# Kernel tuning notes

Measured on AMD Instinct MI355X. Metric: run time of the kernel, lower is better.

Reference implementation:

```python
import jax, jax.numpy as jnp
import numpy as np

B, S, D, H = 2, 2048, 1024, 16
HD = D // H  # head_dim = 64


def _rope(t, cos, sin):
    # t: (B, H, S, HD); cos/sin: (S, HD//2) -> rotate interleaved pairs
    t2 = t.reshape(*t.shape[:-1], HD // 2, 2)
    t1, t2_ = t2[..., 0], t2[..., 1]
    c = cos[None, None, :, :]
    s = sin[None, None, :, :]
    out = jnp.stack([t1 * c - t2_ * s, t1 * s + t2_ * c], axis=-1)
    return out.reshape(t.shape)


def setup_inputs() -> dict:
    key = jax.random.key(0)
    ks = jax.random.split(key, 5)
    x = jax.random.normal(ks[0], (B, S, D), dtype=jnp.float32)
    attn_mask = jnp.tril(jnp.ones((S, S), dtype=bool))  # causal
    # standard RoPE angles: pos * inv_freq
    inv_freq = 1.0 / (10000.0 ** (jnp.arange(0, HD, 2, dtype=jnp.float32) / HD))
    freqs = jnp.arange(S, dtype=jnp.float32)[:, None] * inv_freq[None, :]  # (S, HD//2)
    std = 1.0 / np.sqrt(D)
    w_qkv = jax.random.normal(ks[1], (3 * D, D), dtype=jnp.float32) * std
    b_qkv = jnp.zeros((3 * D,), dtype=jnp.float32)
    w_proj = jax.random.normal(ks[2], (D, D), dtype=jnp.float32) * std
    b_proj = jnp.zeros((D,), dtype=jnp.float32)
    return {"x": x, "attn_mask": attn_mask, "freqs": freqs,
            "w_qkv": w_qkv, "b_qkv": b_qkv, "w_proj": w_proj, "b_proj": b_proj}


def reference(x, attn_mask, freqs, w_qkv, b_qkv, w_proj, b_proj):
    # QKV projection: (B,S,D) -> (B,S,3D), split per einops pattern (three, H, HD)
    qkv = x @ w_qkv.T + b_qkv
    qkv = qkv.reshape(B, S, 3, H, HD)
    q = jnp.transpose(qkv[:, :, 0], (0, 2, 1, 3))  # (B,H,S,HD)
    k = jnp.transpose(qkv[:, :, 1], (0, 2, 1, 3))
    v = jnp.transpose(qkv[:, :, 2], (0, 2, 1, 3))
    cos, sin = jnp.cos(freqs), jnp.sin(freqs)
    q = _rope(q, cos, sin)
    k = _rope(k, cos, sin)
    scale = 1.0 / np.sqrt(HD)
    scores = jnp.einsum("bhqd,bhkd->bhqk", q, k) * scale  # (B,H,S,S)
    scores = jnp.where(attn_mask[None, None, :, :], scores, jnp.finfo(scores.dtype).min)
    attn = jax.nn.softmax(scores, axis=-1)
    out = jnp.einsum("bhqk,bhkd->bhqd", attn, v)  # (B,H,S,HD)
    out = jnp.transpose(out, (0, 2, 1, 3)).reshape(B, S, D)
    return out @ w_proj.T + b_proj
```

## Files before the change

### kernel.cpp

```cpp
#include <hip/hip_runtime.h>

#define S_LEN 2048
#define NH 16
#define HD 64
#define DMODEL 1024

typedef __bf16 bf16x8 __attribute__((ext_vector_type(8)));
typedef float floatx4 __attribute__((ext_vector_type(4)));
typedef short short8 __attribute__((ext_vector_type(8)));

__device__ inline unsigned short f2bf(float f) {
    union { float f; unsigned u; } v; v.f = f;
    unsigned u = v.u;
    unsigned r = (u + 0x7FFFu + ((u >> 16) & 1u)) >> 16;
    return (unsigned short)r;
}

__device__ __forceinline__ void gload_lds16(const void* g, void* l) {
    __builtin_amdgcn_global_load_lds(
        (const __attribute__((address_space(1))) unsigned int*)g,
        (__attribute__((address_space(3))) unsigned int*)l, 16, 0, 0);
}

#define WAITV_BAR(N) do { \
    asm volatile("s_waitcnt vmcnt(" #N ")\n\ts_barrier" ::: "memory"); \
    __builtin_amdgcn_sched_barrier(0); \
} while (0)

__device__ __forceinline__ void cvt4(const float4* __restrict__ src,
                                     uint2* __restrict__ dst, int i) {
    float4 v = src[i];
    union { unsigned short u[4]; uint2 d; } o;
    o.u[0] = f2bf(v.x); o.u[1] = f2bf(v.y); o.u[2] = f2bf(v.z); o.u[3] = f2bf(v.w);
    dst[i] = o.d;
}

__global__ __launch_bounds__(256) void prep_kernel(
    const float* __restrict__ x, const float* __restrict__ wq,
    const float* __restrict__ wp, const float* __restrict__ freqs,
    unsigned short* __restrict__ xb, unsigned short* __restrict__ wqb,
    unsigned short* __restrict__ wpb, float2* __restrict__ cs)
{
    const int tid = blockIdx.x * 256 + threadIdx.x;
    const int nth = gridDim.x * 256;
    for (int i = tid; i < (4096 * 1024) / 4; i += nth) cvt4((const float4*)x, (uint2*)xb, i);
    for (int i = tid; i < (3072 * 1024) / 4; i += nth) cvt4((const float4*)wq, (uint2*)wqb, i);
    for (int i = tid; i < (1024 * 1024) / 4; i += nth) cvt4((const float4*)wp, (uint2*)wpb, i);
    for (int i = tid; i < S_LEN * 32; i += nth) {
        const float f = freqs[i];
        float2 c; c.x = cosf(f); c.y = sinf(f);
        cs[i] = c;
    }
}

#define SROW(r) (((r) & 3) ^ (((r) >> 2) & 3))

#define QKV_STAGE(bi, kk) do { \
    unsigned short* dA_ = smem + (bi) * 8192; \
    unsigned short* dB_ = dA_ + 4096; \
    gload_lds16(ag + (kk),               dA_ + wv * 512); \
    gload_lds16(ag + 64 * DMODEL + (kk), dA_ + 2048 + wv * 512); \
    gload_lds16(bg + (kk),               dB_ + wv * 512); \
    gload_lds16(bg + 64 * DMODEL + (kk), dB_ + 2048 + wv * 512); \
} while (0)

#define QKV_COMPUTE(bi) do { \
    const unsigned short* sA_ = smem + (bi) * 8192; \
    const unsigned short* sB_ = sA_ + 4096; \
    bf16x8 af[4]; \
    _Pragma("unroll") for (int m_ = 0; m_ < 4; m_++) af[m_] = *(const bf16x8*)&sA_[aoff[m_]]; \
    _Pragma("unroll") for (int n_ = 0; n_ < 4; n_++) { \
        bf16x8 bf = *(const bf16x8*)&sB_[boff[n_]]; \
        _Pragma("unroll") for (int m_ = 0; m_ < 4; m_++) \
            acc[m_][n_] = __builtin_amdgcn_mfma_f32_16x16x32_bf16(af[m_], bf, acc[m_][n_], 0, 0, 0); \
    } \
} while (0)

__global__ __launch_bounds__(256, 3) void qkv_gemm_kernel(
    const unsigned short* __restrict__ xb, const unsigned short* __restrict__ wqb,
    const float* __restrict__ bias, const float2* __restrict__ cs,
    unsigned short* __restrict__ qb, unsigned short* __restrict__ kb,
    unsigned short* __restrict__ vb)
{
    __shared__ __align__(16) unsigned short smem[24576];

    const int t = threadIdx.x;
    const int v = (blockIdx.x & 7) * 96 + (blockIdx.x >> 3);
    const int mbase = (v / 24) * 128;
    const int nbase = (v % 24) * 128;
    const int wv = t >> 6, lane = t & 63;
    const int quad = lane >> 4, l16 = lane & 15;
    const int wr = wv >> 1, wc = wv & 1;

    floatx4 acc[4][4];
    #pragma unroll
    for (int m = 0; m < 4; m++)
        #pragma unroll
        for (int n = 0; n < 4; n++)
            #pragma unroll
            for (int r = 0; r < 4; r++) acc[m][n][r] = 0.f;

    const int srow = t >> 2;
    const int schunk = (t & 3) ^ SROW(srow);
    const unsigned short* ag = xb + (size_t)(mbase + srow) * DMODEL + schunk * 8;
    const unsigned short* bg = wqb + (size_t)(nbase + srow) * DMODEL + schunk * 8;

    const int Sl = SROW(l16);
    int aoff[4], boff[4];
    #pragma unroll
    for (int m = 0; m < 4; m++) aoff[m] = (wr * 64 + m * 16 + l16) * 32 + (quad ^ Sl) * 8;
    #pragma unroll
    for (int n = 0; n < 4; n++) boff[n] = (wc * 64 + n * 16 + l16) * 32 + (quad ^ Sl) * 8;

    QKV_STAGE(0, 0);
    QKV_STAGE(1, 32);
    for (int tb = 0; tb < 30; tb += 3) {
        WAITV_BAR(4); QKV_STAGE(2, (tb + 2) * 32); QKV_COMPUTE(0);
        WAITV_BAR(4); QKV_STAGE(0, (tb + 3) * 32); QKV_COMPUTE(1);
        WAITV_BAR(4); QKV_STAGE(1, (tb + 4) * 32); QKV_COMPUTE(2);
    }
    WAITV_BAR(4); QKV_COMPUTE(0);
    WAITV_BAR(0); QKV_COMPUTE(1);

    const int part = nbase >> 10;
    const int bidx = mbase >> 11;
    const int s0   = mbase & 2047;

    if (part == 2) {
        unsigned short* Vt = smem;
        const int hb = (nbase & 1023) >> 6;
        float bvv[4];
        #pragma unroll
        for (int nt = 0; nt < 4; nt++) bvv[nt] = bias[nbase + wc * 64 + nt * 16 + l16];
        #pragma unroll
        for (int shalf = 0; shalf < 2; shalf++) {
            __syncthreads();
            if (wr == shalf) {
                #pragma unroll
                for (int nt = 0; nt < 4; nt++) {
                    const int hdl = wc * 64 + nt * 16 + l16;
                    #pragma unroll
                    for (int m = 0; m < 4; m++)
                        #pragma unroll
                        for (int r = 0; r < 4; r++)
                            Vt[hdl * 72 + m * 16 + quad * 4 + r] = f2bf(acc[m][nt][r] + bvv[nt]);
                }
            }
            __syncthreads();
            const int hdl = t & 127, sp = t >> 7;
            const size_t bh2 = (size_t)bidx * NH + hb + (hdl >> 6);
            #pragma unroll
            for (int c = 0; c < 4; c++) {
                const int sl0 = (sp * 4 + c) * 8;
                const int sg = s0 + shalf * 64 + sl0;
                short8 vv = *(const short8*)&Vt[hdl * 72 + sl0];
                *(short8*)&vb[((bh2 * 256 + (sg >> 3)) * 64 + (hdl & 63)) * 8] = vv;
            }
        }
    } else {
        const size_t bhb = (size_t)bidx * NH;
        const int odd = l16 & 1;
        #pragma unroll
        for (int nt = 0; nt < 4; nt++) {
            const int n_ = nbase + wc * 64 + nt * 16 + l16;
            const int hd = n_ & 63;
            const size_t bh = bhb + ((n_ & 1023) >> 6);
            const float bvv = bias[n_];
            const int ci = (nt * 16 + l16) >> 1;
            #pragma unroll
            for (int m = 0; m < 4; m++) {
                #pragma unroll
                for (int r = 0; r < 4; r++) {
                    const int s = s0 + wr * 64 + m * 16 + quad * 4 + r;
                    float val = acc[m][nt][r] + bvv;
                    float other = __shfl_xor(val, 1, 64);
                    const float2 csv = cs[(size_t)s * 32 + ci];
                    float outv = odd ? fmaf(other, csv.y, val * csv.x)
                                     : fmaf(-other, csv.y, val * csv.x);
                    if (part == 0) {
                        qb[(bh * S_LEN + s) * HD + hd] = f2bf(outv * 0.125f);
                    } else {
                        kb[((bh * 8 + (hd >> 3)) * (size_t)S_LEN + s) * 8 + (hd & 7)] = f2bf(outv);
                    }
                }
            }
        }
    }
}

__global__ __launch_bounds__(512, 4) void attn_kernel(
    const unsigned short* __restrict__ qb, const unsigned short* __restrict__ kb,
    const unsigned short* __restrict__ vbk, unsigned short* __restrict__ ao)
{
    __shared__ __align__(16) unsigned short Ks[2][8 * 512];
    __shared__ __align__(16) unsigned short Vt[2][8 * 512];
    __shared__ __align__(16) unsigned short Pw[8][16 * 72];

    const int t = threadIdx.x;
    const int wv = t >> 6, lane = t & 63, quad = lane >> 4, l16 = lane & 15;
    const int qp = 15 - (blockIdx.x >> 5);
    const int qbase = qp * 128;
    const int bhid = blockIdx.x & 31;
    const int h = bhid & 15, b = bhid >> 4;
    const size_t bh = (size_t)b * NH + h;
    const unsigned short* qg  = qb + bh * S_LEN * HD;
    const unsigned short* kgB = kb + bh * 8 * S_LEN * 8;
    const unsigned short* vgB = vbk + bh * 256 * 64 * 8;

    bf16x8 qf[2];
    {
        const unsigned short* q0 = qg + (size_t)(qbase + wv * 16 + l16) * HD;
        qf[0] = *(const bf16x8*)&q0[quad * 8];
        qf[1] = *(const bf16x8*)&q0[32 + quad * 8];
    }

    bf16x8 ones;
    {
        union { short8 s; bf16x8 v; } o;
        for (int j = 0; j < 8; j++) o.s[j] = 0x3F80;
        ones = o.v;
    }

    floatx4 lfr = {0.f, 0.f, 0.f, 0.f};
    floatx4 Ofr[4];
    for (int nt = 0; nt < 4; nt++)
        for (int r = 0; r < 4; r++) Ofr[nt][r] = 0.f;

    const int ntiles = (qbase >> 6) + 2;

#define ATTN_STAGE(bufi, kt_) do { \
    const int kb_ = (kt_) * 64; \
    const unsigned short* g0 = kgB + ((size_t)wv * S_LEN + kb_ + lane) * 8; \
    gload_lds16(g0, &Ks[bufi][wv * 512]); \
    const unsigned short* g1 = vgB + ((size_t)((kb_ >> 3) + wv) * 64 + lane) * 8; \
    gload_lds16(g1, &Vt[bufi][wv * 512]); \
} while (0)

#define ATTN_COMPUTE(bufi, kt_) do { \
    const int kbase = (kt_) * 64; \
    float pex[4][4]; \
    __builtin_amdgcn_s_setprio(1); \
    _Pragma("unroll") for (int sub = 0; sub < 4; sub++) { \
        bf16x8 kf0 = *(const bf16x8*)&Ks[bufi][(0 * 4 + quad) * 512 + (sub * 16 + l16) * 8]; \
        bf16x8 kf1 = *(const bf16x8*)&Ks[bufi][(1 * 4 + quad) * 512 + (sub * 16 + l16) * 8]; \
        floatx4 sacc = {0.f, 0.f, 0.f, 0.f}; \
        sacc = __builtin_amdgcn_mfma_f32_16x16x32_bf16(kf0, qf[0], sacc, 0, 0, 0); \
        sacc = __builtin_amdgcn_mfma_f32_16x16x32_bf16(kf1, qf[1], sacc, 0, 0, 0); \
        _Pragma("unroll") for (int r = 0; r < 4; r++) pex[sub][r] = sacc[r]; \
    } \
    __builtin_amdgcn_s_setprio(0); \
    if (kbase + 63 > qbase + wv * 16) {            \
        const int q = qbase + wv * 16 + l16; \
        _Pragma("unroll") for (int sub = 0; sub < 4; sub++) \
            _Pragma("unroll") for (int r = 0; r < 4; r++) { \
                const int key = kbase + sub * 16 + quad * 4 + r; \
                if (key > q) pex[sub][r] = -1e30f; \
            } \
    } \
    _Pragma("unroll") for (int sub = 0; sub < 4; sub++) { \
        union { unsigned short s[4]; uint2 u; } pk; \
        _Pragma("unroll") for (int r = 0; r < 4; r++) pk.s[r] = f2bf(__expf(pex[sub][r])); \
        *(uint2*)&Pw[wv][l16 * 72 + sub * 16 + quad * 4] = pk.u; \
    } \
    { \
        bf16x8 pf0 = *(const bf16x8*)&Pw[wv][l16 * 72 + quad * 8]; \
        bf16x8 pf1 = *(const bf16x8*)&Pw[wv][l16 * 72 + 32 + quad * 8]; \
        __builtin_amdgcn_s_setprio(1); \
        lfr = __builtin_amdgcn_mfma_f32_16x16x32_bf16(ones, pf0, lfr, 0, 0, 0); \
        lfr = __builtin_amdgcn_mfma_f32_16x16x32_bf16(ones, pf1, lfr, 0, 0, 0); \
        _Pragma("unroll") for (int nt = 0; nt < 4; nt++) { \
            bf16x8 v0 = *(const bf16x8*)&Vt[bufi][(0 * 4 + quad) * 512 + (nt * 16 + l16) * 8]; \
            bf16x8 v1 = *(const bf16x8*)&Vt[bufi][(1 * 4 + quad) * 512 + (nt * 16 + l16) * 8]; \
            Ofr[nt] = __builtin_amdgcn_mfma_f32_16x16x32_bf16(pf0, v0, Ofr[nt], 0, 0, 0); \
            Ofr[nt] = __builtin_amdgcn_mfma_f32_16x16x32_bf16(pf1, v1, Ofr[nt], 0, 0, 0); \
        } \
        __builtin_amdgcn_s_setprio(0); \
    } \
} while (0)

    ATTN_STAGE(0, 0);
    __syncthreads();
    for (int kt = 0; kt < ntiles; ) {
        if (kt + 1 < ntiles) ATTN_STAGE(1, kt + 1);
        ATTN_COMPUTE(0, kt);
        kt++;
        if (kt >= ntiles) break;
        __syncthreads();
        if (kt + 1 < ntiles) ATTN_STAGE(0, kt + 1);
        ATTN_COMPUTE(1, kt);
        kt++;
        if (kt >= ntiles) break;
        __syncthreads();
    }

    float linv[4];
    #pragma unroll
    for (int r = 0; r < 4; r++) {
        float lq = __shfl(lfr[0], (lane & 48) | (quad * 4 + r), 64);
        linv[r] = 1.f / lq;
    }
    #pragma unroll
    for (int nt = 0; nt < 4; nt++)
        #pragma unroll
        for (int r = 0; r < 4; r++) {
            const int s = qbase + wv * 16 + quad * 4 + r;
            ao[((size_t)b * S_LEN + s) * DMODEL + h * HD + nt * 16 + l16] =
                f2bf(Ofr[nt][r] * linv[r]);
        }
#undef ATTN_STAGE
#undef ATTN_COMPUTE
}

#define PROJ_STAGE(bi, kk) do { \
    unsigned short* dA_ = smem + (bi) * 6144; \
    unsigned short* dB_ = dA_ + 4096; \
    gload_lds16(ag + (kk),               dA_ + wv * 512); \
    gload_lds16(ag + 64 * DMODEL + (kk), dA_ + 2048 + wv * 512); \
    gload_lds16(bg + (kk),               dB_ + wv * 512); \
} while (0)

#define PROJ_COMPUTE(bi) do { \
    const unsigned short* sA_ = smem + (bi) * 6144; \
    const unsigned short* sB_ = sA_ + 4096; \
    bf16x8 af[4]; \
    _Pragma("unroll") for (int m_ = 0; m_ < 4; m_++) af[m_] = *(const bf16x8*)&sA_[aoff[m_]]; \
    _Pragma("unroll") for (int n_ = 0; n_ < 2; n_++) { \
        bf16x8 bf = *(const bf16x8*)&sB_[boff[n_]]; \
        _Pragma("unroll") for (int m_ = 0; m_ < 4; m_++) \
            acc[m_][n_] = __builtin_amdgcn_mfma_f32_16x16x32_bf16(af[m_], bf, acc[m_][n_], 0, 0, 0); \
    } \
} while (0)

__global__ __launch_bounds__(256, 3) void proj_kernel(
    const unsigned short* __restrict__ a, const unsigned short* __restrict__ wpb,
    const float* __restrict__ bias, float* __restrict__ out)
{
    __shared__ __align__(16) unsigned short smem[18432];

    const int t = threadIdx.x;
    const int v = (blockIdx.x & 7) * 64 + (blockIdx.x >> 3);
    const int mbase = (v >> 4) * 128;
    const int nbase = (v & 15) * 64;
    const int wv = t >> 6, lane = t & 63, quad = lane >> 4, l16 = lane & 15;
    const int wr = wv >> 1, wc = wv & 1;

    floatx4 acc[4][2];
    #pragma unroll
    for (int m = 0; m < 4; m++)
        #pragma unroll
        for (int n = 0; n < 2; n++)
            #pragma unroll
            for (int r = 0; r < 4; r++) acc[m][n][r] = 0.f;

    const int srow = t >> 2;
    const int schunk = (t & 3) ^ SROW(srow);
    const unsigned short* ag = a + (size_t)(mbase + srow) * DMODEL + schunk * 8;
    const unsigned short* bg = wpb + (size_t)(nbase + srow) * DMODEL + schunk * 8;

    const int Sl = SROW(l16);
    int aoff[4], boff[2];
    #pragma unroll
    for (int m = 0; m < 4; m++) aoff[m] = (wr * 64 + m * 16 + l16) * 32 + (quad ^ Sl) * 8;
    #pragma unroll
    for (int n = 0; n < 2; n++) boff[n] = (wc * 32 + n * 16 + l16) * 32 + (quad ^ Sl) * 8;

    PROJ_STAGE(0, 0);
    PROJ_STAGE(1, 32);
    for (int tb = 0; tb < 30; tb += 3) {
        WAITV_BAR(3); PROJ_STAGE(2, (tb + 2) * 32); PROJ_COMPUTE(0);
        WAITV_BAR(3); PROJ_STAGE(0, (tb + 3) * 32); PROJ_COMPUTE(1);
        WAITV_BAR(3); PROJ_STAGE(1, (tb + 4) * 32); PROJ_COMPUTE(2);
    }
    WAITV_BAR(3); PROJ_COMPUTE(0);
    WAITV_BAR(0); PROJ_COMPUTE(1);

    #pragma unroll
    for (int n = 0; n < 2; n++) {
        const int nn = nbase + wc * 32 + n * 16 + l16;
        const float bvv = bias[nn];
        #pragma unroll
        for (int m = 0; m < 4; m++)
            #pragma unroll
            for (int r = 0; r < 4; r++)
                out[(size_t)(mbase + wr * 64 + m * 16 + quad * 4 + r) * DMODEL + nn] =
                    acc[m][n][r] + bvv;
    }
}

extern "C" void kernel_launch(void* const* d_in, const int* in_sizes, int n_in,
                              void* d_out, int out_size, void* d_ws, size_t ws_size,
                              hipStream_t stream) {
    const float* x      = (const float*)d_in[0];
    const float* freqs  = (const float*)d_in[2];
    const float* w_qkv  = (const float*)d_in[3];
    const float* b_qkv  = (const float*)d_in[4];
    const float* w_proj = (const float*)d_in[5];
    const float* b_proj = (const float*)d_in[6];
    float* out = (float*)d_out;

    unsigned short* ws = (unsigned short*)d_ws;
    const size_t HSZ = (size_t)2 * NH * S_LEN * HD;
    unsigned short* qb  = ws;
    unsigned short* kb  = ws + HSZ;
    unsigned short* vb  = ws + 2 * HSZ;
    unsigned short* ao  = ws + 3 * HSZ;
    unsigned short* xb  = ws + 4 * HSZ;
    unsigned short* wqb = xb + (size_t)4096 * 1024;
    unsigned short* wpb = wqb + (size_t)3072 * 1024;
    float2* cs = (float2*)(wpb + (size_t)1024 * 1024);

    prep_kernel<<<2048, 256, 0, stream>>>(x, w_qkv, w_proj, freqs, xb, wqb, wpb, cs);
    qkv_gemm_kernel<<<768, 256, 0, stream>>>(xb, wqb, b_qkv, cs, qb, kb, vb);
    attn_kernel<<<512, 512, 0, stream>>>(qb, kb, vb, ao);
    proj_kernel<<<512, 256, 0, stream>>>(ao, wpb, b_proj, out);
}
```

Before: 200.6 us.

## Load GEMM weight operand directly into registers and use double-buffered LDS for activations

In both the QKV and output-projection GEMMs, the weight (B) operand is no longer staged through LDS but is loaded straight from global memory into MFMA-ready register fragments, with a register double buffer. Only the activation (A) tile still goes through LDS, now in a two-slot buffer synchronised with __syncthreads in place of the triple-buffered vmcnt/barrier pipeline. This cuts LDS footprint and LDS read traffic for B, which could allow higher occupancy. The cost is uncoalesced 16-byte per-lane global loads of B that may be fetched redundantly by both wave rows, plus a weaker latency-hiding pipeline that relies on the compiler's waitcnt insertion.

Result: slower. 230.0 us (+14.7%).

```diff
diff --git a/kernel.cpp b/kernel.cpp
--- a/kernel.cpp
+++ b/kernel.cpp
@@ -21,11 +21,6 @@
         (const __attribute__((address_space(1))) unsigned int*)g,
         (__attribute__((address_space(3))) unsigned int*)l, 16, 0, 0);
 }
-
-#define WAITV_BAR(N) do { \
-    asm volatile("s_waitcnt vmcnt(" #N ")\n\ts_barrier" ::: "memory"); \
-    __builtin_amdgcn_sched_barrier(0); \
-} while (0)
 
 __device__ __forceinline__ void cvt4(const float4* __restrict__ src,
                                      uint2* __restrict__ dst, int i) {
@@ -55,24 +50,22 @@
 
 #define SROW(r) (((r) & 3) ^ (((r) >> 2) & 3))
 
-#define QKV_STAGE(bi, kk) do { \
-    unsigned short* dA_ = smem + (bi) * 8192; \
-    unsigned short* dB_ = dA_ + 4096; \
-    gload_lds16(ag + (kk),               dA_ + wv * 512); \
-    gload_lds16(ag + 64 * DMODEL + (kk), dA_ + 2048 + wv * 512); \
-    gload_lds16(bg + (kk),               dB_ + wv * 512); \
-    gload_lds16(bg + 64 * DMODEL + (kk), dB_ + 2048 + wv * 512); \
-} while (0)
-
-#define QKV_COMPUTE(bi) do { \
-    const unsigned short* sA_ = smem + (bi) * 8192; \
-    const unsigned short* sB_ = sA_ + 4096; \
+#define QKV_STAGE(dA, kk) do { \
+    gload_lds16(ag + (kk),               (dA) + wv * 512); \
+    gload_lds16(ag + 64 * DMODEL + (kk), (dA) + 2048 + wv * 512); \
+} while (0)
+
+#define QKV_BLOAD(BF, kk) do { \
+    _Pragma("unroll") for (int n_ = 0; n_ < 4; n_++) \
+        (BF)[n_] = *(const bf16x8*)(bqb + (size_t)n_ * 16 * DMODEL + (kk)); \
+} while (0)
+
+#define QKV_COMPUTE(sA, BF) do { \
     bf16x8 af[4]; \
-    _Pragma("unroll") for (int m_ = 0; m_ < 4; m_++) af[m_] = *(const bf16x8*)&sA_[aoff[m_]]; \
+    _Pragma("unroll") for (int m_ = 0; m_ < 4; m_++) af[m_] = *(const bf16x8*)&(sA)[aoff[m_]]; \
     _Pragma("unroll") for (int n_ = 0; n_ < 4; n_++) { \
-        bf16x8 bf = *(const bf16x8*)&sB_[boff[n_]]; \
         _Pragma("unroll") for (int m_ = 0; m_ < 4; m_++) \
-            acc[m_][n_] = __builtin_amdgcn_mfma_f32_16x16x32_bf16(af[m_], bf, acc[m_][n_], 0, 0, 0); \
+            acc[m_][n_] = __builtin_amdgcn_mfma_f32_16x16x32_bf16(af[m_], (BF)[n_], acc[m_][n_], 0, 0, 0); \
     } \
 } while (0)
 
@@ -82,7 +75,9 @@
     unsigned short* __restrict__ qb, unsigned short* __restrict__ kb,
     unsigned short* __restrict__ vb)
 {
-    __shared__ __align__(16) unsigned short smem[24576];
+    __shared__ __align__(16) unsigned short smem[9216];
+    unsigned short* A0 = smem;
+    unsigned short* A1 = smem + 4096;
 
     const int t = threadIdx.x;
     const int v = (blockIdx.x & 7) * 96 + (blockIdx.x >> 3);
@@ -103,24 +98,30 @@
     const int srow = t >> 2;
     const int schunk = (t & 3) ^ SROW(srow);
     const unsigned short* ag = xb + (size_t)(mbase + srow) * DMODEL + schunk * 8;
-    const unsigned short* bg = wqb + (size_t)(nbase + srow) * DMODEL + schunk * 8;
+
+    const unsigned short* bqb = wqb + (size_t)(nbase + wc * 64 + l16) * DMODEL + quad * 8;
 
     const int Sl = SROW(l16);
-    int aoff[4], boff[4];
+    int aoff[4];
     #pragma unroll
     for (int m = 0; m < 4; m++) aoff[m] = (wr * 64 + m * 16 + l16) * 32 + (quad ^ Sl) * 8;
-    #pragma unroll
-    for (int n = 0; n < 4; n++) boff[n] = (wc * 64 + n * 16 + l16) * 32 + (quad ^ Sl) * 8;
-
-    QKV_STAGE(0, 0);
-    QKV_STAGE(1, 32);
-    for (int tb = 0; tb < 30; tb += 3) {
-        WAITV_BAR(4); QKV_STAGE(2, (tb + 2) * 32); QKV_COMPUTE(0);
-        WAITV_BAR(4); QKV_STAGE(0, (tb + 3) * 32); QKV_COMPUTE(1);
-        WAITV_BAR(4); QKV_STAGE(1, (tb + 4) * 32); QKV_COMPUTE(2);
-    }
-    WAITV_BAR(4); QKV_COMPUTE(0);
-    WAITV_BAR(0); QKV_COMPUTE(1);
+
+    bf16x8 bfc[4], bfn[4];
+    QKV_STAGE(A0, 0);
+    QKV_BLOAD(bfc, 0);
+    __syncthreads();
+    for (int k0 = 0; k0 < DMODEL; k0 += 64) {
+        QKV_STAGE(A1, k0 + 32);
+        QKV_BLOAD(bfn, k0 + 32);
+        QKV_COMPUTE(A0, bfc);
+        __syncthreads();
+        if (k0 + 64 < DMODEL) {
+            QKV_STAGE(A0, k0 + 64);
+            QKV_BLOAD(bfc, k0 + 64);
+        }
+        QKV_COMPUTE(A1, bfn);
+        __syncthreads();
+    }
 
     const int part = nbase >> 10;
     const int bidx = mbase >> 11;
@@ -311,23 +312,22 @@
 #undef ATTN_COMPUTE
 }
 
-#define PROJ_STAGE(bi, kk) do { \
-    unsigned short* dA_ = smem + (bi) * 6144; \
-    unsigned short* dB_ = dA_ + 4096; \
-    gload_lds16(ag + (kk),               dA_ + wv * 512); \
-    gload_lds16(ag + 64 * DMODEL + (kk), dA_ + 2048 + wv * 512); \
-    gload_lds16(bg + (kk),               dB_ + wv * 512); \
-} while (0)
-
-#define PROJ_COMPUTE(bi) do { \
-    const unsigned short* sA_ = smem + (bi) * 6144; \
-    const unsigned short* sB_ = sA_ + 4096; \
+#define PROJ_STAGE(dA, kk) do { \
+    gload_lds16(ag + (kk),               (dA) + wv * 512); \
+    gload_lds16(ag + 64 * DMODEL + (kk), (dA) + 2048 + wv * 512); \
+} while (0)
+
+#define PROJ_BLOAD(BF, kk) do { \
+    _Pragma("unroll") for (int n_ = 0; n_ < 2; n_++) \
+        (BF)[n_] = *(const bf16x8*)(bqb + (size_t)n_ * 16 * DMODEL + (kk)); \
+} while (0)
+
+#define PROJ_COMPUTE(sA, BF) do { \
     bf16x8 af[4]; \
-    _Pragma("unroll") for (int m_ = 0; m_ < 4; m_++) af[m_] = *(const bf16x8*)&sA_[aoff[m_]]; \
+    _Pragma("unroll") for (int m_ = 0; m_ < 4; m_++) af[m_] = *(const bf16x8*)&(sA)[aoff[m_]]; \
     _Pragma("unroll") for (int n_ = 0; n_ < 2; n_++) { \
-        bf16x8 bf = *(const bf16x8*)&sB_[boff[n_]]; \
         _Pragma("unroll") for (int m_ = 0; m_ < 4; m_++) \
-            acc[m_][n_] = __builtin_amdgcn_mfma_f32_16x16x32_bf16(af[m_], bf, acc[m_][n_], 0, 0, 0); \
+            acc[m_][n_] = __builtin_amdgcn_mfma_f32_16x16x32_bf16(af[m_], (BF)[n_], acc[m_][n_], 0, 0, 0); \
     } \
 } while (0)
 
@@ -335,7 +335,9 @@
     const unsigned short* __restrict__ a, const unsigned short* __restrict__ wpb,
     const float* __restrict__ bias, float* __restrict__ out)
 {
-    __shared__ __align__(16) unsigned short smem[18432];
+    __shared__ __align__(16) unsigned short smem[8192];
+    unsigned short* A0 = smem;
+    unsigned short* A1 = smem + 4096;
 
     const int t = threadIdx.x;
     const int v = (blockIdx.x & 7) * 64 + (blockIdx.x >> 3);
@@ -355,24 +357,29 @@
     const int srow = t >> 2;
     const int schunk = (t & 3) ^ SROW(srow);
     const unsigned short* ag = a + (size_t)(mbase + srow) * DMODEL + schunk * 8;
-    const unsigned short* bg = wpb + (size_t)(nbase + srow) * DMODEL + schunk * 8;
+    const unsigned short* bqb = wpb + (size_t)(nbase + wc * 32 + l16) * DMODEL + quad * 8;
 
     const int Sl = SROW(l16);
-    int aoff[4], boff[2];
+    int aoff[4];
     #pragma unroll
     for (int m = 0; m < 4; m++) aoff[m] = (wr * 64 + m * 16 + l16) * 32 + (quad ^ Sl) * 8;
-    #pragma unroll
-    for (int n = 0; n < 2; n++) boff[n] = (wc * 32 + n * 16 + l16) * 32 + (quad ^ Sl) * 8;
-
-    PROJ_STAGE(0, 0);
-    PROJ_STAGE(1, 32);
-    for (int tb = 0; tb < 30; tb += 3) {
-        WAITV_BAR(3); PROJ_STAGE(2, (tb + 2) * 32); PROJ_COMPUTE(0);
-        WAITV_BAR(3); PROJ_STAGE(0, (tb + 3) * 32); PROJ_COMPUTE(1);
-        WAITV_BAR(3); PROJ_STAGE(1, (tb + 4) * 32); PROJ_COMPUTE(2);
-    }
-    WAITV_BAR(3); PROJ_COMPUTE(0);
-    WAITV_BAR(0); PROJ_COMPUTE(1);
+
+    bf16x8 bfc[2], bfn[2];
+    PROJ_STAGE(A0, 0);
+    PROJ_BLOAD(bfc, 0);
+    __syncthreads();
+    for (int k0 = 0; k0 < DMODEL; k0 += 64) {
+        PROJ_STAGE(A1, k0 + 32);
+        PROJ_BLOAD(bfn, k0 + 32);
+        PROJ_COMPUTE(A0, bfc);
+        __syncthreads();
+        if (k0 + 64 < DMODEL) {
+            PROJ_STAGE(A0, k0 + 64);
+            PROJ_BLOAD(bfc, k0 + 64);
+        }
+        PROJ_COMPUTE(A1, bfn);
+        __syncthreads();
+    }
 
     #pragma unroll
     for (int n = 0; n < 2; n++) {
```
